# Kernel tuning notes

Hardware: AMD Instinct MI355X
Metric: run time of the kernel (lower is better)

The kernel has to match this reference:

```python
import jax, jax.numpy as jnp
import numpy as np

D_MODEL = 1024
NUM_HEADS = 16
HDIM = D_MODEL // NUM_HEADS
THETA = 10000.0


def setup_inputs() -> dict:
    key = jax.random.key(0)
    ks = jax.random.split(key, 5)
    bs, seq = 4, 2048
    std = np.sqrt(2.0 / (D_MODEL + D_MODEL))
    def w(k):
        # trunc_normal approximated by clipped normal (same distribution family)
        return jnp.clip(std * jax.random.normal(k, (D_MODEL, D_MODEL), jnp.float32), -3 * std, 3 * std)
    return {
        "x": jax.random.normal(ks[0], (bs, seq, D_MODEL), jnp.float32),
        "Wq": w(ks[1]), "Wk": w(ks[2]), "Wv": w(ks[3]), "Wo": w(ks[4]),
        "token_positions": jnp.arange(seq, dtype=jnp.int64),
    }


def _rope(x, token_positions):
    # x: (bs, H, S, hdim); rotate even/odd interleaved pairs
    inv_freq = THETA ** (-2.0 * jnp.arange(HDIM // 2, dtype=jnp.float32) / HDIM)
    freqs = token_positions.astype(jnp.float32)[:, None] * inv_freq[None, :]  # (S, hdim/2)
    cos, sin = jnp.cos(freqs), jnp.sin(freqs)
    x_even, x_odd = x[..., 0::2], x[..., 1::2]
    out_even = x_even * cos - x_odd * sin
    out_odd = x_odd * cos + x_even * sin
    # interleave back: stack on new last axis then reshape
    return jnp.stack([out_even, out_odd], axis=-1).reshape(x.shape)


def reference(x, Wq, Wk, Wv, Wo, token_positions):
    bs, seq, _ = x.shape
    q = (x @ Wq.T).reshape(bs, seq, NUM_HEADS, HDIM).transpose(0, 2, 1, 3)
    k = (x @ Wk.T).reshape(bs, seq, NUM_HEADS, HDIM).transpose(0, 2, 1, 3)
    v = (x @ Wv.T).reshape(bs, seq, NUM_HEADS, HDIM).transpose(0, 2, 1, 3)
    q = _rope(q, token_positions)
    k = _rope(k, token_positions)
    scores = jnp.einsum("bhsd,bhtd->bhst", q, k) / jnp.sqrt(jnp.float32(HDIM))
    mask = jnp.tril(jnp.ones((seq, seq), dtype=bool))
    scores = jnp.where(mask, scores, -jnp.inf)
    attn = jax.nn.softmax(scores, axis=-1)
    out = jnp.einsum("bhst,bhtd->bhsd", attn, v)
    out = out.transpose(0, 2, 1, 3).reshape(bs, seq, D_MODEL)
    return out @ Wo.T
```

## Files before the change

### kernel.cpp

```cpp
#include <hip/hip_runtime.h>
#include <hip/hip_fp16.h>

typedef _Float16 half8 __attribute__((ext_vector_type(8)));
typedef _Float16 half4 __attribute__((ext_vector_type(4)));
typedef _Float16 half2v __attribute__((ext_vector_type(2)));
typedef float f32x4 __attribute__((ext_vector_type(4)));
typedef float f32x8v __attribute__((ext_vector_type(8)));
typedef float f32x16 __attribute__((ext_vector_type(16)));

#define SEQ   2048
#define DM    1024
#define NH    16
#define HD    64
#define BSZ   4

#if __has_builtin(__builtin_amdgcn_exp2f)
#define EXP2(x) __builtin_amdgcn_exp2f(x)
#else
#define EXP2(x) exp2f(x)
#endif

#define QSCALE 0.1803368801f
#define ROPE_C 0.41524101186f

__device__ __forceinline__ void gload16(const void* g, void* l) {
  __builtin_amdgcn_global_load_lds((const __attribute__((address_space(1))) void*)g,
                                   (__attribute__((address_space(3))) void*)l,
                                   16, 0, 0);
}

__global__ void cvt4(const float* __restrict__ src, _Float16* __restrict__ dst, int n4) {
  int i = blockIdx.x * blockDim.x + threadIdx.x;
  if (i < n4) {
    float4 v = ((const float4*)src)[i];
    half4 o = { (_Float16)v.x, (_Float16)v.y, (_Float16)v.z, (_Float16)v.w };
    ((half4*)dst)[i] = o;
  }
}

__global__ void cvtW(const float* __restrict__ s0, const float* __restrict__ s1,
                     const float* __restrict__ s2, const float* __restrict__ s3,
                     _Float16* __restrict__ dqkv, _Float16* __restrict__ dO) {
  const int y = blockIdx.y;
  const float* src = (y == 0) ? s0 : (y == 1) ? s1 : (y == 2) ? s2 : s3;
  _Float16* dst = (y < 3) ? (dqkv + (long)y * (1u << 20)) : dO;
  int i = blockIdx.x * blockDim.x + threadIdx.x;
  float4 v = ((const float4*)src)[i];
  half4 o = { (_Float16)v.x, (_Float16)v.y, (_Float16)v.z, (_Float16)v.w };
  ((half4*)dst)[i] = o;
}

template<int MODE>
__global__ __launch_bounds__(256)
void gemm_hk(const _Float16* __restrict__ A, const _Float16* __restrict__ B,
             _Float16* __restrict__ oQ, _Float16* __restrict__ oK,
             _Float16* __restrict__ oVt, float* __restrict__ oF,
             const int* __restrict__ tp) {
  __shared__ _Float16 As[3][128*32];
  __shared__ _Float16 Bs[3][128*32];
  const int tid  = threadIdx.x;
  const int wid  = tid >> 6, lane = tid & 63;
  const int wm   = wid >> 1, wn = wid & 1;
  const int fr   = lane & 15, fg = lane >> 4;
  const long m0  = (long)blockIdx.x * 128;
  const long n0  = (long)blockIdx.y * 128;
  const int lrow = lane >> 2;
  const int lcol = (lane & 3) * 8;
  const _Float16* ga0 = A + (m0 + wid*32 + lrow) * 1024 + lcol;
  const _Float16* gb0 = B + (n0 + wid*32 + lrow) * 1024 + lcol;
  const int lofs = wid*32*32;

  f32x4 acc[4][4] = {};

  gload16(ga0,                &As[0][lofs]);
  gload16(ga0 + 16*1024,      &As[0][lofs + 16*32]);
  gload16(gb0,                &Bs[0][lofs]);
  gload16(gb0 + 16*1024,      &Bs[0][lofs + 16*32]);
  gload16(ga0 + 32,           &As[1][lofs]);
  gload16(ga0 + 32 + 16*1024, &As[1][lofs + 16*32]);
  gload16(gb0 + 32,           &Bs[1][lofs]);
  gload16(gb0 + 32 + 16*1024, &Bs[1][lofs + 16*32]);

  int cur = 0;
  for (int k0 = 0; k0 < 992; k0 += 32) {
    asm volatile("s_waitcnt vmcnt(4)" ::: "memory");
    __builtin_amdgcn_s_barrier();

    if (k0 + 64 < 1024) {
      int wr = cur + 2; if (wr >= 3) wr -= 3;
      gload16(ga0 + k0 + 64,           &As[wr][lofs]);
      gload16(ga0 + k0 + 64 + 16*1024, &As[wr][lofs + 16*32]);
      gload16(gb0 + k0 + 64,           &Bs[wr][lofs]);
      gload16(gb0 + k0 + 64 + 16*1024, &Bs[wr][lofs + 16*32]);
    }

    half8 af[4], bf[4];
#pragma unroll
    for (int i = 0; i < 4; ++i) {
      af[i] = *(const half8*)&As[cur][(wm*64 + i*16 + fr)*32 + fg*8];
      bf[i] = *(const half8*)&Bs[cur][(wn*64 + i*16 + fr)*32 + fg*8];
    }
    __builtin_amdgcn_s_setprio(1);
#pragma unroll
    for (int i = 0; i < 4; ++i)
#pragma unroll
      for (int j = 0; j < 4; ++j)
        acc[i][j] = __builtin_amdgcn_mfma_f32_16x16x32_f16(af[i], bf[j], acc[i][j], 0, 0, 0);
    __builtin_amdgcn_s_setprio(0);

    cur += 1; if (cur >= 3) cur -= 3;
  }

  {
    asm volatile("s_waitcnt vmcnt(0)" ::: "memory");
    __builtin_amdgcn_s_barrier();
    half8 af[4], bf[4];
#pragma unroll
    for (int i = 0; i < 4; ++i) {
      af[i] = *(const half8*)&As[cur][(wm*64 + i*16 + fr)*32 + fg*8];
      bf[i] = *(const half8*)&Bs[cur][(wn*64 + i*16 + fr)*32 + fg*8];
    }
    __builtin_amdgcn_s_setprio(1);
#pragma unroll
    for (int i = 0; i < 4; ++i)
#pragma unroll
      for (int j = 0; j < 4; ++j)
        acc[i][j] = __builtin_amdgcn_mfma_f32_16x16x32_f16(af[i], bf[j], acc[i][j], 0, 0, 0);
    __builtin_amdgcn_s_setprio(0);
  }

  if (MODE == 0) {
    const int which = (int)(n0 >> 10);
    const int nloc0 = ((int)n0 & 1023) + wn*64;
    const bool odd = fr & 1;
#pragma unroll
    for (int i = 0; i < 4; ++i) {
      const long r0 = m0 + wm*64 + i*16 + fg*4;
      const int  bb = (int)(r0 >> 11);
      const int  s  = (int)(r0 & 2047);
#pragma unroll
      for (int j = 0; j < 4; ++j) {
        const int nl = nloc0 + j*16 + fr;
        const int h  = nl >> 6, d = nl & 63;
        const long bh = (long)(bb*NH + h);
        if (which == 2) {
          half4 pk = { (_Float16)acc[i][j][0], (_Float16)acc[i][j][1],
                       (_Float16)acc[i][j][2], (_Float16)acc[i][j][3] };
          *(half4*)&oVt[(bh*HD + d)*SEQ + s] = pk;
        } else {
          const float inv = exp2f(-ROPE_C * (float)(d >> 1));
#pragma unroll
          for (int r = 0; r < 4; ++r) {
            const float v = acc[i][j][r];
            const float p = __shfl_xor(v, 1);
            float sn, cs;
            __sincosf((float)tp[s + r] * inv, &sn, &cs);
            const float out = odd ? (v*cs + p*sn) : (v*cs - p*sn);
            if (which == 0)
              oQ[(bh*SEQ + s + r)*HD + d] = (_Float16)(out * QSCALE);
            else
              oK[(bh*SEQ + s + r)*HD + d] = (_Float16)out;
          }
        }
      }
    }
  } else {
#pragma unroll
    for (int i = 0; i < 4; ++i) {
      const long r0 = m0 + wm*64 + i*16 + fg*4;
#pragma unroll
      for (int j = 0; j < 4; ++j) {
        const long col = n0 + wn*64 + j*16 + fr;
#pragma unroll
        for (int r = 0; r < 4; ++r)
          oF[(r0 + r)*DM + col] = acc[i][j][r];
      }
    }
  }
}

__global__ __launch_bounds__(256, 2)
void fattn(const _Float16* __restrict__ Q, const _Float16* __restrict__ K,
           const _Float16* __restrict__ Vt, _Float16* __restrict__ O) {
  __shared__ _Float16 Ks[2][64*64];
  __shared__ _Float16 Vs[2][64*64];
  const int tid = threadIdx.x, wid = tid >> 6, lane = tid & 63;
  const int q31 = lane & 31, hi = lane >> 5;
  const int qp  = (q31 & 19) | ((q31 & 4) << 1) | ((q31 & 8) >> 1);
  const int bh = blockIdx.x, b = bh >> 4, h = bh & 15;
  const int y = blockIdx.y;
  const int qs_[2] = { (15 - y)*128 + wid*32, y*128 + wid*32 };
  const _Float16* Qb = Q + (long)bh * SEQ * HD;
  const _Float16* Kb = K + (long)bh * SEQ * HD;
  const _Float16* Vb = Vt + (long)bh * HD * SEQ;

  half8 qf[2][4];
#pragma unroll
  for (int s = 0; s < 2; ++s)
#pragma unroll
    for (int c = 0; c < 4; ++c)
      qf[s][c] = *(const half8*)&Qb[(qs_[s] + q31)*HD + c*16 + hi*8];

  f32x16 oacc[2][2] = {};
  float m_s[2] = { -1e30f, -1e30f }, l_s[2] = { 0.f, 0.f };

  const int srow = lane >> 3;
  const int sc16 = (lane & 7) ^ srow;
  const int r1 = wid*16 + srow, r2 = r1 + 8;

  const int nt = (15 - y)*2 + 2;

  gload16(Kb + (long)r1*HD + sc16*8, &Ks[0][(wid*16)*64]);
  gload16(Kb + (long)r2*HD + sc16*8, &Ks[0][(wid*16 + 8)*64]);
  gload16(Vb + (long)r1*SEQ + sc16*8, &Vs[0][(wid*16)*64]);
  gload16(Vb + (long)r2*SEQ + sc16*8, &Vs[0][(wid*16 + 8)*64]);
  __syncthreads();

  int cur = 0;
  for (int t = 0; t < nt; ++t) {
    const int kv0 = t * 64;

    if (t + 1 < nt) {
      const int nkv = kv0 + 64;
      gload16(Kb + (long)(nkv + r1)*HD + sc16*8, &Ks[cur^1][(wid*16)*64]);
      gload16(Kb + (long)(nkv + r2)*HD + sc16*8, &Ks[cur^1][(wid*16 + 8)*64]);
      gload16(Vb + (long)r1*SEQ + nkv + sc16*8,  &Vs[cur^1][(wid*16)*64]);
      gload16(Vb + (long)r2*SEQ + nkv + sc16*8,  &Vs[cur^1][(wid*16 + 8)*64]);
    }

    const char* Kc = (const char*)&Ks[cur][0];
    const char* Vc = (const char*)&Vs[cur][0];

#pragma unroll
    for (int hh = 0; hh < 2; ++hh) {
      const int kvb = kv0 + 32*hh;
#pragma unroll
      for (int s = 0; s < 2; ++s) {
        const int qs0 = qs_[s];
        if (kvb > qs0 + 31) continue;

        f32x16 sa = {};
        __builtin_amdgcn_s_setprio(1);
#pragma unroll
        for (int c = 0; c < 4; ++c) {
          const int row = 32*hh + qp;
          const half8 kf = *(const half8*)(Kc + row*128 + ((c*32 + hi*16) ^ ((row & 7) << 4)));
          sa = __builtin_amdgcn_mfma_f32_32x32x16_f16(kf, qf[s][c], sa, 0, 0, 0);
        }
        __builtin_amdgcn_s_setprio(0);

        if (kvb + 31 > qs0) {
          const int thr = qs0 + q31 - kvb - 8*hi;
#pragma unroll
          for (int r = 0; r < 16; ++r) {
            const int cr = (r & 3) + 4*((r >> 2) & 1) + 16*(r >> 3);
            if (cr > thr) sa[r] = -1e30f;
          }
        }

        f32x8v mx8;
#pragma unroll
        for (int i = 0; i < 8; ++i) mx8[i] = fmaxf(sa[i], sa[i+8]);
        f32x4 mx4;
#pragma unroll
        for (int i = 0; i < 4; ++i) mx4[i] = fmaxf(mx8[i], mx8[i+4]);
        float pm = fmaxf(fmaxf(mx4[0], mx4[1]), fmaxf(mx4[2], mx4[3]));
        pm = fmaxf(pm, __shfl_xor(pm, 32));

        if (!__all(pm <= m_s[s] + 8.0f)) {
          const float mn = fmaxf(m_s[s], pm);
          const float fac = EXP2(m_s[s] - mn);
          m_s[s] = mn;
          l_s[s] *= fac;
          oacc[s][0] *= fac;
          oacc[s][1] *= fac;
        }
        const float mrow = m_s[s];

#pragma unroll
        for (int r = 0; r < 16; ++r) sa[r] = EXP2(sa[r] - mrow);

        f32x8v s8;
#pragma unroll
        for (int i = 0; i < 8; ++i) s8[i] = sa[i] + sa[i+8];
        f32x4 s4v;
#pragma unroll
        for (int i = 0; i < 4; ++i) s4v[i] = s8[i] + s8[i+4];
        float ps = (s4v[0] + s4v[1]) + (s4v[2] + s4v[3]);
        ps += __shfl_xor(ps, 32);
        l_s[s] += ps;

        half8 pf0, pf1;
#pragma unroll
        for (int g = 0; g < 4; ++g) {
          half2v t0 = (half2v)__builtin_amdgcn_cvt_pkrtz(sa[2*g],   sa[2*g+1]);
          half2v t1 = (half2v)__builtin_amdgcn_cvt_pkrtz(sa[8+2*g], sa[8+2*g+1]);
          pf0[2*g]   = t0[0];  pf0[2*g+1] = t0[1];
          pf1[2*g]   = t1[0];  pf1[2*g+1] = t1[1];
        }

        __builtin_amdgcn_s_setprio(1);
#pragma unroll
        for (int ks = 0; ks < 2; ++ks) {
          const half8 pf = ks ? pf1 : pf0;
#pragma unroll
          for (int nd = 0; nd < 2; ++nd) {
            const int row = nd*32 + q31;
            const half8 vf = *(const half8*)(Vc + row*128 +
                              ((hh*64 + ks*32 + hi*16) ^ ((row & 7) << 4)));
            oacc[s][nd] = __builtin_amdgcn_mfma_f32_32x32x16_f16(vf, pf, oacc[s][nd], 0, 0, 0);
          }
        }
        __builtin_amdgcn_s_setprio(0);
      }
    }

    __syncthreads();
    cur ^= 1;
  }

#pragma unroll
  for (int s = 0; s < 2; ++s) {
    const float rl = __builtin_amdgcn_rcpf(l_s[s]);
    _Float16* orow = O + ((long)b*SEQ + (qs_[s] + q31))*DM + h*64;
#pragma unroll
    for (int nd = 0; nd < 2; ++nd)
#pragma unroll
      for (int g = 0; g < 4; ++g) {
        half2v lo  = (half2v)__builtin_amdgcn_cvt_pkrtz(oacc[s][nd][4*g+0]*rl, oacc[s][nd][4*g+1]*rl);
        half2v hi2 = (half2v)__builtin_amdgcn_cvt_pkrtz(oacc[s][nd][4*g+2]*rl, oacc[s][nd][4*g+3]*rl);
        half4 o4 = __builtin_shufflevector(lo, hi2, 0, 1, 2, 3);
        *(half4*)&orow[nd*32 + g*8 + 4*hi] = o4;
      }
  }
}

extern "C" void kernel_launch(void* const* d_in, const int* in_sizes, int n_in,
                              void* d_out, int out_size, void* d_ws, size_t ws_size,
                              hipStream_t stream) {
  const float* x  = (const float*)d_in[0];
  const float* Wq = (const float*)d_in[1];
  const float* Wk = (const float*)d_in[2];
  const float* Wv = (const float*)d_in[3];
  const float* Wo = (const float*)d_in[4];
  const int*   tp = (const int*)d_in[5];
  float* out = (float*)d_out;

  char* ws = (char*)d_ws;
  _Float16* xh   = (_Float16*)(ws);
  _Float16* Wqkv = (_Float16*)(ws + (16u << 20));
  _Float16* Woh  = (_Float16*)(ws + (22u << 20));
  _Float16* Qb   = (_Float16*)(ws + (24u << 20));
  _Float16* Kb   = (_Float16*)(ws + (40u << 20));
  _Float16* Vtb  = (_Float16*)(ws + (56u << 20));
  _Float16* attn = (_Float16*)(ws + (72u << 20));

  cvt4<<<8192, 256, 0, stream>>>(x, xh, 2097152);
  cvtW<<<dim3(1024, 4), 256, 0, stream>>>(Wq, Wk, Wv, Wo, Wqkv, Woh);

  gemm_hk<0><<<dim3(64, 24), 256, 0, stream>>>(xh, Wqkv, Qb, Kb, Vtb, nullptr, tp);
  fattn<<<dim3(64, 8), 256, 0, stream>>>(Qb, Kb, Vtb, attn);
  gemm_hk<1><<<dim3(64, 8), 256, 0, stream>>>(attn, Woh, nullptr, nullptr, nullptr, out, nullptr);
}
```

Baseline: 174.0 us.

## Widen QKV GEMM tile to 128x256 and XOR-swizzle LDS staging

Makes the GEMM's N tile a template parameter: the QKV projection now uses 256-wide tiles (half the grid), so each A tile loaded from global memory is reused across twice as many output columns. It also changes how global loads map to LDS, using an XOR swizzle on 16-byte chunks, and reads fragments through a matching swizzled address to cut LDS bank conflicts. The wider tile doubles accumulator registers and B-tile LDS per block, which may lower occupancy. The smaller grid (768 blocks) may also fill the CUs less evenly.

```diff
diff --git a/kernel.cpp b/kernel.cpp
--- a/kernel.cpp
+++ b/kernel.cpp
@@ -56,55 +56,70 @@
              _Float16* __restrict__ oQ, _Float16* __restrict__ oK,
              _Float16* __restrict__ oVt, float* __restrict__ oF,
              const int* __restrict__ tp) {
+  constexpr int BN    = (MODE == 0) ? 256 : 128;
+  constexpr int NW    = BN / 2;
+  constexpr int NF    = NW / 16;
+  constexpr int BROWS = BN / 4;
+  constexpr int NBL   = BROWS / 16;
   __shared__ _Float16 As[3][128*32];
-  __shared__ _Float16 Bs[3][128*32];
+  __shared__ _Float16 Bs[3][BN*32];
   const int tid  = threadIdx.x;
   const int wid  = tid >> 6, lane = tid & 63;
   const int wm   = wid >> 1, wn = wid & 1;
   const int fr   = lane & 15, fg = lane >> 4;
   const long m0  = (long)blockIdx.x * 128;
-  const long n0  = (long)blockIdx.y * 128;
-  const int lrow = lane >> 2;
-  const int lcol = (lane & 3) * 8;
-  const _Float16* ga0 = A + (m0 + wid*32 + lrow) * 1024 + lcol;
-  const _Float16* gb0 = B + (n0 + wid*32 + lrow) * 1024 + lcol;
-  const int lofs = wid*32*32;
-
-  f32x4 acc[4][4] = {};
-
-  gload16(ga0,                &As[0][lofs]);
-  gload16(ga0 + 16*1024,      &As[0][lofs + 16*32]);
-  gload16(gb0,                &Bs[0][lofs]);
-  gload16(gb0 + 16*1024,      &Bs[0][lofs + 16*32]);
-  gload16(ga0 + 32,           &As[1][lofs]);
-  gload16(ga0 + 32 + 16*1024, &As[1][lofs + 16*32]);
-  gload16(gb0 + 32,           &Bs[1][lofs]);
-  gload16(gb0 + 32 + 16*1024, &Bs[1][lofs + 16*32]);
+  const long n0  = (long)blockIdx.y * BN;
+  const int sg    = (lane & 7) ^ ((lane >> 3) & 7);
+  const int srowl = 2*(lane >> 3) + (sg >> 2);
+  const int scol  = (sg & 3) * 8;
+  const _Float16* ga0 = A + (m0 + wid*32 + srowl) * 1024 + scol;
+  const _Float16* gb0 = B + (n0 + wid*BROWS + srowl) * 1024 + scol;
+  const int lofsA = wid*32*32;
+  const int lofsB = wid*BROWS*32;
+
+  f32x4 acc[4][NF] = {};
+
+  auto stage = [&](int buf, int k) {
+    gload16(ga0 + k,           &As[buf][lofsA]);
+    gload16(ga0 + k + 16*1024, &As[buf][lofsA + 16*32]);
+#pragma unroll
+    for (int r = 0; r < NBL; ++r)
+      gload16(gb0 + k + r*16*1024, &Bs[buf][lofsB + r*16*32]);
+  };
+  auto ldfrag = [&](const char* base, int R) -> half8 {
+    const int r = R & 31, r2 = r >> 1;
+    return *(const half8*)(base + (R >> 5)*2048 + r2*128 +
+                           (((((r & 1) << 2) | fg) ^ (r2 & 7)) << 4));
+  };
+
+  stage(0, 0);
+  stage(1, 32);
 
   int cur = 0;
   for (int k0 = 0; k0 < 992; k0 += 32) {
-    asm volatile("s_waitcnt vmcnt(4)" ::: "memory");
+    if constexpr (MODE == 0)
+      asm volatile("s_waitcnt vmcnt(6)" ::: "memory");
+    else
+      asm volatile("s_waitcnt vmcnt(4)" ::: "memory");
     __builtin_amdgcn_s_barrier();
 
     if (k0 + 64 < 1024) {
       int wr = cur + 2; if (wr >= 3) wr -= 3;
-      gload16(ga0 + k0 + 64,           &As[wr][lofs]);
-      gload16(ga0 + k0 + 64 + 16*1024, &As[wr][lofs + 16*32]);
-      gload16(gb0 + k0 + 64,           &Bs[wr][lofs]);
-      gload16(gb0 + k0 + 64 + 16*1024, &Bs[wr][lofs + 16*32]);
-    }
-
-    half8 af[4], bf[4];
-#pragma unroll
-    for (int i = 0; i < 4; ++i) {
-      af[i] = *(const half8*)&As[cur][(wm*64 + i*16 + fr)*32 + fg*8];
-      bf[i] = *(const half8*)&Bs[cur][(wn*64 + i*16 + fr)*32 + fg*8];
-    }
+      stage(wr, k0 + 64);
+    }
+
+    const char* Ab = (const char*)&As[cur][0];
+    const char* Bb = (const char*)&Bs[cur][0];
+    half8 af[4], bf[NF];
+#pragma unroll
+    for (int i = 0; i < 4; ++i)  af[i] = ldfrag(Ab, wm*64 + i*16 + fr);
+#pragma unroll
+    for (int j = 0; j < NF; ++j) bf[j] = ldfrag(Bb, wn*NW + j*16 + fr);
     __builtin_amdgcn_s_setprio(1);
 #pragma unroll
     for (int i = 0; i < 4; ++i)
 #pragma unroll
-      for (int j = 0; j < 4; ++j)
+      for (int j = 0; j < NF; ++j)
         acc[i][j] = __builtin_amdgcn_mfma_f32_16x16x32_f16(af[i], bf[j], acc[i][j], 0, 0, 0);
     __builtin_amdgcn_s_setprio(0);
 
@@ -114,24 +129,25 @@
   {
     asm volatile("s_waitcnt vmcnt(0)" ::: "memory");
     __builtin_amdgcn_s_barrier();
-    half8 af[4], bf[4];
-#pragma unroll
-    for (int i = 0; i < 4; ++i) {
-      af[i] = *(const half8*)&As[cur][(wm*64 + i*16 + fr)*32 + fg*8];
-      bf[i] = *(const half8*)&Bs[cur][(wn*64 + i*16 + fr)*32 + fg*8];
-    }
+    const char* Ab = (const char*)&As[cur][0];
+    const char* Bb = (const char*)&Bs[cur][0];
+    half8 af[4], bf[NF];
+#pragma unroll
+    for (int i = 0; i < 4; ++i)  af[i] = ldfrag(Ab, wm*64 + i*16 + fr);
+#pragma unroll
+    for (int j = 0; j < NF; ++j) bf[j] = ldfrag(Bb, wn*NW + j*16 + fr);
     __builtin_amdgcn_s_setprio(1);
 #pragma unroll
     for (int i = 0; i < 4; ++i)
 #pragma unroll
-      for (int j = 0; j < 4; ++j)
+      for (int j = 0; j < NF; ++j)
         acc[i][j] = __builtin_amdgcn_mfma_f32_16x16x32_f16(af[i], bf[j], acc[i][j], 0, 0, 0);
     __builtin_amdgcn_s_setprio(0);
   }
 
   if (MODE == 0) {
     const int which = (int)(n0 >> 10);
-    const int nloc0 = ((int)n0 & 1023) + wn*64;
+    const int nloc0 = ((int)n0 & 1023) + wn*NW;
     const bool odd = fr & 1;
 #pragma unroll
     for (int i = 0; i < 4; ++i) {
@@ -139,7 +155,7 @@
       const int  bb = (int)(r0 >> 11);
       const int  s  = (int)(r0 & 2047);
 #pragma unroll
-      for (int j = 0; j < 4; ++j) {
+      for (int j = 0; j < NF; ++j) {
         const int nl = nloc0 + j*16 + fr;
         const int h  = nl >> 6, d = nl & 63;
         const long bh = (long)(bb*NH + h);
@@ -169,8 +185,8 @@
     for (int i = 0; i < 4; ++i) {
       const long r0 = m0 + wm*64 + i*16 + fg*4;
 #pragma unroll
-      for (int j = 0; j < 4; ++j) {
-        const long col = n0 + wn*64 + j*16 + fr;
+      for (int j = 0; j < NF; ++j) {
+        const long col = n0 + wn*NW + j*16 + fr;
 #pragma unroll
         for (int r = 0; r < 4; ++r)
           oF[(r0 + r)*DM + col] = acc[i][j][r];
@@ -358,7 +374,7 @@
   cvt4<<<8192, 256, 0, stream>>>(x, xh, 2097152);
   cvtW<<<dim3(1024, 4), 256, 0, stream>>>(Wq, Wk, Wv, Wo, Wqkv, Woh);
 
-  gemm_hk<0><<<dim3(64, 24), 256, 0, stream>>>(xh, Wqkv, Qb, Kb, Vtb, nullptr, tp);
+  gemm_hk<0><<<dim3(64, 12), 256, 0, stream>>>(xh, Wqkv, Qb, Kb, Vtb, nullptr, tp);
   fattn<<<dim3(64, 8), 256, 0, stream>>>(Qb, Kb, Vtb, attn);
   gemm_hk<1><<<dim3(64, 8), 256, 0, stream>>>(attn, Woh, nullptr, nullptr, nullptr, out, nullptr);
 }
```

Result: slower. 179.3 us (+3.0%).
